# Kernel optimization log

Hardware: AMD Instinct MI355X
Metric: run time of the kernel (lower is better)

## Reference

```python
import jax, jax.numpy as jnp
import numpy as np

NUM_UNIQUE = 256     # number of distinct edge types (static)
STRENGTH = 0.01      # regularizer strength (init kwarg)


def setup_inputs() -> dict:
    key = jax.random.key(0)
    k1, k2, k3 = jax.random.split(key, 3)
    E = 33554432  # 2^25 synapses
    x = jax.random.normal(k1, (E,), dtype=jnp.float32)
    idx = jax.random.randint(k2, (E,), 0, NUM_UNIQUE, dtype=jnp.int32)
    target_mean = jax.random.normal(k3, (NUM_UNIQUE,), dtype=jnp.float32)
    return {"x": x, "idx": idx, "target_mean": target_mean}


def reference(x, idx, target_mean):
    # unsorted_segment_mean: scatter-add of values and counts per edge type
    seg_sum = jax.ops.segment_sum(x, idx, num_segments=NUM_UNIQUE)
    seg_cnt = jax.ops.segment_sum(jnp.ones_like(x), idx, num_segments=NUM_UNIQUE)
    mean_w = seg_sum / jnp.maximum(seg_cnt, 1.0)  # TF yields 0 for empty segments
    dev = mean_w - target_mean
    reg_loss = jnp.mean(jnp.square(dev))
    return reg_loss * jnp.float32(STRENGTH)
```

## Files before the change

### kernel.cpp

```cpp
#include <hip/hip_runtime.h>
#include <hip/hip_bf16.h>

#define NBINS 256
#define NCOPIES 4
#define STRENGTH 0.01f

#define CNT_SHIFT 41
#define FP_SCALE 524288.0f
#define FP_INV_SCALE (1.0 / 524288.0)
#define FP_BIAS (1 << 23)

__device__ __forceinline__ unsigned long long pack_elem(float x) {
    int v = __float2int_rn(x * FP_SCALE) + FP_BIAS;
    v = min(max(v, 0), (1 << 24) - 1);
    return (1ULL << CNT_SHIFT) | (unsigned long long)(unsigned int)v;
}

__global__ __launch_bounds__(1024) void seg_hist_kernel(
    const float4* __restrict__ x4,
    const int4* __restrict__ idx4,
    float* __restrict__ gsum,
    unsigned int* __restrict__ gcnt,
    int nvec)
{
    __shared__ unsigned long long h[NCOPIES][NBINS];

    for (int i = threadIdx.x; i < NCOPIES * NBINS; i += blockDim.x)
        ((unsigned long long*)h)[i] = 0ull;
    __syncthreads();

    unsigned long long* hist = h[(threadIdx.x >> 6) & (NCOPIES - 1)];

    const int stride = gridDim.x * blockDim.x;
    for (int i = blockIdx.x * blockDim.x + threadIdx.x; i < nvec; i += stride) {
        const float4 xv = x4[i];
        const int4  iv = idx4[i];
        atomicAdd(&hist[iv.x], pack_elem(xv.x));
        atomicAdd(&hist[iv.y], pack_elem(xv.y));
        atomicAdd(&hist[iv.z], pack_elem(xv.z));
        atomicAdd(&hist[iv.w], pack_elem(xv.w));
    }
    __syncthreads();

    for (int b = threadIdx.x; b < NBINS; b += blockDim.x) {
        unsigned long long p = h[0][b] + h[1][b] + h[2][b] + h[3][b];
        unsigned int cnt = (unsigned int)(p >> CNT_SHIFT);
        long long lowsum = (long long)(p & ((1ULL << CNT_SHIFT) - 1))
                         - (long long)cnt * FP_BIAS;
        if (cnt) {
            float s = (float)((double)lowsum * FP_INV_SCALE);
            atomicAdd(&gsum[b], s);
            atomicAdd(&gcnt[b], cnt);
        }
    }
}

__global__ __launch_bounds__(NBINS) void finalize_kernel(
    const float* __restrict__ gsum,
    const unsigned int* __restrict__ gcnt,
    const float* __restrict__ target,
    float* __restrict__ out)
{
    const int t = threadIdx.x;
    const float s = gsum[t];
    const float c = (float)gcnt[t];
    const float mean = s / fmaxf(c, 1.0f);
    const float dev = mean - target[t];
    float v = dev * dev;

    #pragma unroll
    for (int off = 32; off > 0; off >>= 1) {
        v += __shfl_down(v, off, 64);
    }
    __shared__ float red[4];
    if ((t & 63) == 0) red[t >> 6] = v;
    __syncthreads();
    if (t == 0) {
        const float tot = red[0] + red[1] + red[2] + red[3];
        out[0] = tot * (STRENGTH / (float)NBINS);
    }
}

extern "C" void kernel_launch(void* const* d_in, const int* in_sizes, int n_in,
                              void* d_out, int out_size, void* d_ws, size_t ws_size,
                              hipStream_t stream)
{
    const float* x      = (const float*)d_in[0];
    const int*   idx    = (const int*)d_in[1];
    const float* target = (const float*)d_in[2];
    float*       out    = (float*)d_out;

    const int E    = in_sizes[0];
    const int nvec = E / 4;

    float*        gsum = (float*)d_ws;
    unsigned int* gcnt = (unsigned int*)(gsum + NBINS);

    hipMemsetAsync(d_ws, 0, NBINS * (sizeof(float) + sizeof(unsigned int)), stream);

    const int block = 1024;
    const int grid  = 512;
    seg_hist_kernel<<<grid, block, 0, stream>>>(
        (const float4*)x, (const int4*)idx, gsum, gcnt, nvec);

    finalize_kernel<<<1, NBINS, 0, stream>>>(gsum, gcnt, target, out);
}
```

Baseline: 280.0 us.

## Replace packed 64-bit LDS histogram with per-wave float sum and count histograms

Drops the fixed-point packing of sum and count into one 64-bit LDS atomic. Instead it keeps separate 32-bit float-sum and uint-count histograms, one copy per wave (16 copies). The main loop is also unrolled to two float4/int4 loads per iteration to raise memory-level parallelism. This removes the pack arithmetic and 64-bit atomics and cuts contention between waves. In exchange it doubles the number of LDS atomic operations per element, and summation order now depends on float atomic ordering.

```diff
diff --git a/kernel.cpp b/kernel.cpp
--- a/kernel.cpp
+++ b/kernel.cpp
@@ -1,20 +1,8 @@
 #include <hip/hip_runtime.h>
-#include <hip/hip_bf16.h>
 
 #define NBINS 256
-#define NCOPIES 4
+#define NWAVES 16
 #define STRENGTH 0.01f
-
-#define CNT_SHIFT 41
-#define FP_SCALE 524288.0f
-#define FP_INV_SCALE (1.0 / 524288.0)
-#define FP_BIAS (1 << 23)
-
-__device__ __forceinline__ unsigned long long pack_elem(float x) {
-    int v = __float2int_rn(x * FP_SCALE) + FP_BIAS;
-    v = min(max(v, 0), (1 << 24) - 1);
-    return (1ULL << CNT_SHIFT) | (unsigned long long)(unsigned int)v;
-}
 
 __global__ __launch_bounds__(1024) void seg_hist_kernel(
     const float4* __restrict__ x4,
@@ -23,35 +11,68 @@
     unsigned int* __restrict__ gcnt,
     int nvec)
 {
-    __shared__ unsigned long long h[NCOPIES][NBINS];
+    __shared__ float        hsum[NWAVES][NBINS];
+    __shared__ unsigned int hcnt[NWAVES][NBINS];
 
-    for (int i = threadIdx.x; i < NCOPIES * NBINS; i += blockDim.x)
-        ((unsigned long long*)h)[i] = 0ull;
+    for (int i = threadIdx.x; i < NWAVES * NBINS; i += blockDim.x) {
+        ((float*)hsum)[i] = 0.0f;
+        ((unsigned int*)hcnt)[i] = 0u;
+    }
     __syncthreads();
 
-    unsigned long long* hist = h[(threadIdx.x >> 6) & (NCOPIES - 1)];
+    const int w = (threadIdx.x >> 6) & (NWAVES - 1);
+    float*        hs = hsum[w];
+    unsigned int* hc = hcnt[w];
 
-    const int stride = gridDim.x * blockDim.x;
-    for (int i = blockIdx.x * blockDim.x + threadIdx.x; i < nvec; i += stride) {
-        const float4 xv = x4[i];
-        const int4  iv = idx4[i];
-        atomicAdd(&hist[iv.x], pack_elem(xv.x));
-        atomicAdd(&hist[iv.y], pack_elem(xv.y));
-        atomicAdd(&hist[iv.z], pack_elem(xv.z));
-        atomicAdd(&hist[iv.w], pack_elem(xv.w));
+    const int stride  = gridDim.x * blockDim.x;
+    const int stride2 = stride << 1;
+
+    for (int i = blockIdx.x * blockDim.x + threadIdx.x; i < nvec; i += stride2) {
+        const float4 xa = x4[i];
+        const int4   ia = idx4[i];
+        const int j = i + stride;
+        if (j < nvec) {
+            const float4 xb = x4[j];
+            const int4   ib = idx4[j];
+            atomicAdd(&hs[ia.x], xa.x);
+            atomicAdd(&hs[ia.y], xa.y);
+            atomicAdd(&hs[ia.z], xa.z);
+            atomicAdd(&hs[ia.w], xa.w);
+            atomicAdd(&hs[ib.x], xb.x);
+            atomicAdd(&hs[ib.y], xb.y);
+            atomicAdd(&hs[ib.z], xb.z);
+            atomicAdd(&hs[ib.w], xb.w);
+            atomicAdd(&hc[ia.x], 1u);
+            atomicAdd(&hc[ia.y], 1u);
+            atomicAdd(&hc[ia.z], 1u);
+            atomicAdd(&hc[ia.w], 1u);
+            atomicAdd(&hc[ib.x], 1u);
+            atomicAdd(&hc[ib.y], 1u);
+            atomicAdd(&hc[ib.z], 1u);
+            atomicAdd(&hc[ib.w], 1u);
+        } else {
+            atomicAdd(&hs[ia.x], xa.x);
+            atomicAdd(&hs[ia.y], xa.y);
+            atomicAdd(&hs[ia.z], xa.z);
+            atomicAdd(&hs[ia.w], xa.w);
+            atomicAdd(&hc[ia.x], 1u);
+            atomicAdd(&hc[ia.y], 1u);
+            atomicAdd(&hc[ia.z], 1u);
+            atomicAdd(&hc[ia.w], 1u);
+        }
     }
     __syncthreads();
 
     for (int b = threadIdx.x; b < NBINS; b += blockDim.x) {
-        unsigned long long p = h[0][b] + h[1][b] + h[2][b] + h[3][b];
-        unsigned int cnt = (unsigned int)(p >> CNT_SHIFT);
-        long long lowsum = (long long)(p & ((1ULL << CNT_SHIFT) - 1))
-                         - (long long)cnt * FP_BIAS;
-        if (cnt) {
-            float s = (float)((double)lowsum * FP_INV_SCALE);
-            atomicAdd(&gsum[b], s);
-            atomicAdd(&gcnt[b], cnt);
+        float        s = 0.0f;
+        unsigned int c = 0u;
+        #pragma unroll
+        for (int w2 = 0; w2 < NWAVES; ++w2) {
+            s += hsum[w2][b];
+            c += hcnt[w2][b];
         }
+        atomicAdd(&gsum[b], s);
+        atomicAdd(&gcnt[b], c);
     }
 }
 
```

Result: slower. 363.2 us (+29.7%).

## Offload one of four elements per vector to global-memory atomic histograms

Applied to the files above, without the earlier changes.

Routes one element of each float4 to one of 32 global packed 64-bit histogram copies via global atomics, leaving three elements on the shared-memory (LDS) atomics. The aim is to relieve LDS atomic contention by spreading the work across the L2 atomic units. The finalize kernel sums the 32 global copies and merges them with the per-block results. Global atomics to only 32x256 addresses from many blocks may contend heavily in L2 and could be slower than LDS.

```diff
diff --git a/kernel.cpp b/kernel.cpp
--- a/kernel.cpp
+++ b/kernel.cpp
@@ -1,19 +1,20 @@
 #include <hip/hip_runtime.h>
-#include <hip/hip_bf16.h>
 
 #define NBINS 256
 #define NCOPIES 4
+#define NCOPY_G 32
 #define STRENGTH 0.01f
 
-#define CNT_SHIFT 41
+#define CNT_SHIFT_L 41
+#define CNT_SHIFT_G 45
 #define FP_SCALE 524288.0f
 #define FP_INV_SCALE (1.0 / 524288.0)
 #define FP_BIAS (1 << 23)
 
-__device__ __forceinline__ unsigned long long pack_elem(float x) {
+__device__ __forceinline__ unsigned int fp_elem(float x) {
     int v = __float2int_rn(x * FP_SCALE) + FP_BIAS;
     v = min(max(v, 0), (1 << 24) - 1);
-    return (1ULL << CNT_SHIFT) | (unsigned long long)(unsigned int)v;
+    return (unsigned int)v;
 }
 
 __global__ __launch_bounds__(1024) void seg_hist_kernel(
@@ -21,6 +22,7 @@
     const int4* __restrict__ idx4,
     float* __restrict__ gsum,
     unsigned int* __restrict__ gcnt,
+    unsigned long long* __restrict__ gbuf,
     int nvec)
 {
     __shared__ unsigned long long h[NCOPIES][NBINS];
@@ -30,22 +32,23 @@
     __syncthreads();
 
     unsigned long long* hist = h[(threadIdx.x >> 6) & (NCOPIES - 1)];
+    unsigned long long* gcopy = gbuf + (blockIdx.x & (NCOPY_G - 1)) * NBINS;
 
     const int stride = gridDim.x * blockDim.x;
     for (int i = blockIdx.x * blockDim.x + threadIdx.x; i < nvec; i += stride) {
         const float4 xv = x4[i];
         const int4  iv = idx4[i];
-        atomicAdd(&hist[iv.x], pack_elem(xv.x));
-        atomicAdd(&hist[iv.y], pack_elem(xv.y));
-        atomicAdd(&hist[iv.z], pack_elem(xv.z));
-        atomicAdd(&hist[iv.w], pack_elem(xv.w));
+        atomicAdd(&gcopy[iv.w], (1ULL << CNT_SHIFT_G) | (unsigned long long)fp_elem(xv.w));
+        atomicAdd(&hist[iv.x], (1ULL << CNT_SHIFT_L) | (unsigned long long)fp_elem(xv.x));
+        atomicAdd(&hist[iv.y], (1ULL << CNT_SHIFT_L) | (unsigned long long)fp_elem(xv.y));
+        atomicAdd(&hist[iv.z], (1ULL << CNT_SHIFT_L) | (unsigned long long)fp_elem(xv.z));
     }
     __syncthreads();
 
     for (int b = threadIdx.x; b < NBINS; b += blockDim.x) {
         unsigned long long p = h[0][b] + h[1][b] + h[2][b] + h[3][b];
-        unsigned int cnt = (unsigned int)(p >> CNT_SHIFT);
-        long long lowsum = (long long)(p & ((1ULL << CNT_SHIFT) - 1))
+        unsigned int cnt = (unsigned int)(p >> CNT_SHIFT_L);
+        long long lowsum = (long long)(p & ((1ULL << CNT_SHIFT_L) - 1))
                          - (long long)cnt * FP_BIAS;
         if (cnt) {
             float s = (float)((double)lowsum * FP_INV_SCALE);
@@ -58,12 +61,24 @@
 __global__ __launch_bounds__(NBINS) void finalize_kernel(
     const float* __restrict__ gsum,
     const unsigned int* __restrict__ gcnt,
+    const unsigned long long* __restrict__ gbuf,
     const float* __restrict__ target,
     float* __restrict__ out)
 {
     const int t = threadIdx.x;
-    const float s = gsum[t];
-    const float c = (float)gcnt[t];
+
+    unsigned long long p = 0ull;
+    #pragma unroll
+    for (int c = 0; c < NCOPY_G; ++c)
+        p += gbuf[c * NBINS + t];
+
+    unsigned int cnt_g = (unsigned int)(p >> CNT_SHIFT_G);
+    long long low_g = (long long)(p & ((1ULL << CNT_SHIFT_G) - 1))
+                    - (long long)cnt_g * FP_BIAS;
+    const float s_g = (float)((double)low_g * FP_INV_SCALE);
+
+    const float s = gsum[t] + s_g;
+    const float c = (float)(gcnt[t] + cnt_g);
     const float mean = s / fmaxf(c, 1.0f);
     const float dev = mean - target[t];
     float v = dev * dev;
@@ -93,15 +108,19 @@
     const int E    = in_sizes[0];
     const int nvec = E / 4;
 
-    float*        gsum = (float*)d_ws;
-    unsigned int* gcnt = (unsigned int*)(gsum + NBINS);
+    float*              gsum = (float*)d_ws;
+    unsigned int*       gcnt = (unsigned int*)(gsum + NBINS);
+    unsigned long long* gbuf = (unsigned long long*)(gcnt + NBINS);
 
-    hipMemsetAsync(d_ws, 0, NBINS * (sizeof(float) + sizeof(unsigned int)), stream);
+    hipMemsetAsync(d_ws, 0,
+                   NBINS * (sizeof(float) + sizeof(unsigned int))
+                   + NCOPY_G * NBINS * sizeof(unsigned long long),
+                   stream);
 
     const int block = 1024;
     const int grid  = 512;
     seg_hist_kernel<<<grid, block, 0, stream>>>(
-        (const float4*)x, (const int4*)idx, gsum, gcnt, nvec);
+        (const float4*)x, (const int4*)idx, gsum, gcnt, gbuf, nvec);
 
-    finalize_kernel<<<1, NBINS, 0, stream>>>(gsum, gcnt, target, out);
+    finalize_kernel<<<1, NBINS, 0, stream>>>(gsum, gcnt, gbuf, target, out);
 }
```

Measured after the change: 443.5 us. +58.4%, slower.
